# Kernel optimization log

Hardware: AMD Instinct MI355X
Metric: run time of the kernel (lower is better)

## Reference

```python
import jax, jax.numpy as jnp
import numpy as np

B = 16384          # batch_size
NF = 50            # n_fields
K = 16             # embedding_dim
V = 1_000_000      # input_dim (vocab)
H = 400            # fc hidden
NNZ = B * NF


def _xavier(key, shape):
    fan_in, fan_out = shape
    lim = (6.0 / (fan_in + fan_out)) ** 0.5
    return jax.random.uniform(key, shape, minval=-lim, maxval=lim, dtype=jnp.float32)


def setup_inputs() -> dict:
    key = jax.random.key(0)
    ks = jax.random.split(key, 12)
    feats = jax.random.randint(ks[0], (NNZ,), 0, V)
    # n_fields contiguous features per sample (required by view(batch_size,-1))
    index = jnp.repeat(jnp.arange(B), NF)
    values = jax.random.uniform(ks[1], (NNZ,), dtype=jnp.float32)
    bias = jnp.zeros((1, 1), jnp.float32)
    weights = _xavier(ks[2], (V, 1))
    embedding = _xavier(ks[3], (V, K))
    d = NF * K  # 800
    W0 = _xavier(ks[4], (d, H))
    b0 = jax.random.normal(ks[5], (1, 1), jnp.float32)
    W1 = _xavier(ks[6], (H, H))
    b1 = jax.random.normal(ks[7], (1, 1), jnp.float32)
    W2 = _xavier(ks[8], (H, 1))
    b2 = jax.random.normal(ks[9], (1, 1), jnp.float32)
    return dict(index=index, feats=feats, values=values, bias=bias,
                weights=weights, embedding=embedding,
                W0=W0, b0=b0, W1=W1, b1=b1, W2=W2, b2=b2, batch_size=B)


def reference(index, feats, values, bias, weights, embedding,
              W0, b0, W1, b1, W2, b2, batch_size):
    # gather (F.embedding)
    w = weights[feats, 0]              # [nnz]
    emb = embedding[feats]             # [nnz, K]

    # first order: segment-sum of w*v, plus bias ([B] + [1,1] -> [1,B], as in torch)
    first = jax.ops.segment_sum(w * values, index, num_segments=batch_size) + bias

    # second order: FM pooling trick, fused over all K dims in one segment reduce
    ev = emb * values[:, None]                                        # [nnz, K]
    s1 = jax.ops.segment_sum(ev, index, num_segments=batch_size)      # [B, K]
    s2 = jax.ops.segment_sum(ev * ev, index, num_segments=batch_size) # [B, K]
    second = 0.5 * jnp.sum(s1 * s1 - s2, axis=1)                      # [B]

    # higher order MLP (relu on every layer, scalar biases)
    x = emb.reshape(batch_size, -1)    # [B, NF*K]
    x = jax.nn.relu(x @ W0 + b0)
    x = jax.nn.relu(x @ W1 + b1)
    x = jax.nn.relu(x @ W2 + b2)       # [B, 1]
    higher = x.reshape(-1)             # [B]

    return jax.nn.sigmoid(first + second + higher)  # [1, B]
```

## Files before the change

kernel.cpp:

```cpp
#include <hip/hip_runtime.h>
#include <hip/hip_bf16.h>


#define BATCH 16384
#define NFLD  50
#define EK    16
#define DDIM  800
#define HDIM  400
#define HPAD  416
#define NPAD  512

typedef __attribute__((ext_vector_type(8))) __bf16 bf16x8;
typedef __attribute__((ext_vector_type(4))) float  f32x4;

typedef const __attribute__((address_space(1))) unsigned int* gas_u32p;
typedef __attribute__((address_space(3))) unsigned int*       las_u32p;

__device__ __forceinline__ void gld_lds16(const void* g, void* l) {
    __builtin_amdgcn_global_load_lds((gas_u32p)g, (las_u32p)l, 16, 0, 0);
}

__global__ __launch_bounds__(256) void transpose_pad_kernel(
    const float* __restrict__ src, __hip_bfloat16* __restrict__ dst,
    int srcK, int srcN, int dstCols)
{
    __shared__ float tile[32][33];
    const int tx = threadIdx.x & 31, ty = threadIdx.x >> 5;
    const int k0 = blockIdx.x * 32, n0 = blockIdx.y * 32;
#pragma unroll
    for (int r = 0; r < 4; ++r) {
        int k = k0 + ty + r * 8;
        int n = n0 + tx;
        float v = (k < srcK && n < srcN) ? src[(long)k * srcN + n] : 0.f;
        tile[ty + r * 8][tx] = v;
    }
    __syncthreads();
#pragma unroll
    for (int r = 0; r < 4; ++r) {
        int n = n0 + ty + r * 8;
        int k = k0 + tx;
        dst[(long)n * dstCols + k] = __float2bfloat16(tile[tx][ty + r * 8]);
    }
}

__global__ __launch_bounds__(256) void gather_fm_kernel(
    const int* __restrict__ feats, const float* __restrict__ values,
    const float* __restrict__ biasp, const float* __restrict__ weights,
    const float* __restrict__ embedding,
    float* __restrict__ fs, __hip_bfloat16* __restrict__ x)
{
    const int wave = threadIdx.x >> 6;
    const int lane = threadIdx.x & 63;
    const int s    = blockIdx.x * 4 + wave;
    const int r    = lane >> 2, c = lane & 3;
    const long base = (long)s * NFLD;

    int   f = 0; float v = 0.f, wsum = 0.f;
    if (lane < NFLD) {
        f = feats[base + lane];
        v = values[base + lane];
        wsum = weights[f] * v;
    }

    f32x4 s1 = {0.f, 0.f, 0.f, 0.f}, s2 = {0.f, 0.f, 0.f, 0.f};
#pragma unroll
    for (int p = 0; p < 4; ++p) {
        const int j = p * 16 + r;
        if (p < 3 || r < 2) {
            int   fj = __shfl(f, j);
            float vj = __shfl(v, j);
            const float4 e = *(const float4*)(embedding + (long)fj * EK + c * 4);
            f32x4 ef = {e.x, e.y, e.z, e.w};
            f32x4 ev = ef * vj;
            s1 += ev;
            s2 += ev * ev;
            __hip_bfloat16 pk[4] = {
                __float2bfloat16(e.x), __float2bfloat16(e.y),
                __float2bfloat16(e.z), __float2bfloat16(e.w)};
            *(uint2*)&x[(long)s * DDIM + j * EK + c * 4] = *(uint2*)pk;
        }
    }
#pragma unroll
    for (int m = 4; m <= 32; m <<= 1) {
        s1.x += __shfl_xor(s1.x, m); s1.y += __shfl_xor(s1.y, m);
        s1.z += __shfl_xor(s1.z, m); s1.w += __shfl_xor(s1.w, m);
        s2.x += __shfl_xor(s2.x, m); s2.y += __shfl_xor(s2.y, m);
        s2.z += __shfl_xor(s2.z, m); s2.w += __shfl_xor(s2.w, m);
    }
    float t = (s1.x * s1.x - s2.x) + (s1.y * s1.y - s2.y)
            + (s1.z * s1.z - s2.z) + (s1.w * s1.w - s2.w);
    t += __shfl_xor(t, 1); t += __shfl_xor(t, 2);
    wsum += __shfl_xor(wsum, 1);  wsum += __shfl_xor(wsum, 2);
    wsum += __shfl_xor(wsum, 4);  wsum += __shfl_xor(wsum, 8);
    wsum += __shfl_xor(wsum, 16); wsum += __shfl_xor(wsum, 32);
    if (lane == 0) fs[s] = wsum + 0.5f * t + biasp[0];
}

template <int KDIM, bool OUT_BF16, int LDC, bool PAD_OUT>
__global__ __launch_bounds__(256) void gemm_relu_kernel(
    const __hip_bfloat16* __restrict__ A,
    const __hip_bfloat16* __restrict__ Bt,
    const float* __restrict__ biasp,
    void* __restrict__ C)
{
    constexpr int KT = KDIM / 32;
    __shared__ __align__(16) __hip_bfloat16 sA[128 * 32];
    __shared__ __align__(16) __hip_bfloat16 sB[128 * 32];

    const int tid  = threadIdx.x;
    const int wave = tid >> 6, lane = tid & 63;
    const int l16  = lane & 15, quad = lane >> 4;
    const int waveM = wave & 1, waveN = wave >> 1;
    const int m0 = blockIdx.y * 128;
    const int n0 = blockIdx.x * 128;

    f32x4 acc[4][4] = {};

    const long ar0 = (long)(m0 + wave * 16 + (lane >> 2)) * KDIM;
    const long ar1 = ar0 + (long)64 * KDIM;
    const long br0 = (long)(n0 + wave * 16 + (lane >> 2)) * KDIM;
    const long br1 = br0 + (long)64 * KDIM;
    const int  ac  = (lane & 3) * 8;
    __hip_bfloat16* ldsA0 = sA + wave * 512 + lane * 8;
    __hip_bfloat16* ldsA1 = sA + 2048 + wave * 512 + lane * 8;
    __hip_bfloat16* ldsB0 = sB + wave * 512 + lane * 8;
    __hip_bfloat16* ldsB1 = sB + 2048 + wave * 512 + lane * 8;

    for (int kt = 0; kt < KT; ++kt) {
        const int k0 = kt * 32;
        gld_lds16(A  + ar0 + k0 + ac, ldsA0);
        gld_lds16(A  + ar1 + k0 + ac, ldsA1);
        gld_lds16(Bt + br0 + k0 + ac, ldsB0);
        gld_lds16(Bt + br1 + k0 + ac, ldsB1);
        __syncthreads();

        bf16x8 af[4], bfr[4];
#pragma unroll
        for (int i = 0; i < 4; ++i)
            af[i] = *(const bf16x8*)&sA[(waveM * 64 + i * 16 + l16) * 32 + quad * 8];
#pragma unroll
        for (int j = 0; j < 4; ++j)
            bfr[j] = *(const bf16x8*)&sB[(waveN * 64 + j * 16 + l16) * 32 + quad * 8];
#pragma unroll
        for (int i = 0; i < 4; ++i)
#pragma unroll
            for (int j = 0; j < 4; ++j)
                acc[i][j] = __builtin_amdgcn_mfma_f32_16x16x32_bf16(
                    af[i], bfr[j], acc[i][j], 0, 0, 0);
        __syncthreads();
    }

    const float bias = biasp[0];
#pragma unroll
    for (int i = 0; i < 4; ++i) {
        const int row = m0 + waveM * 64 + i * 16 + quad * 4;
#pragma unroll
        for (int j = 0; j < 4; ++j) {
            const int col = n0 + waveN * 64 + j * 16 + l16;
#pragma unroll
            for (int r = 0; r < 4; ++r) {
                float v = acc[i][j][r] + bias;
                v = v > 0.f ? v : 0.f;
                if constexpr (OUT_BF16) {
                    __hip_bfloat16* Cp = (__hip_bfloat16*)C;
                    if (col < HDIM)
                        Cp[(long)(row + r) * LDC + col] = __float2bfloat16(v);
                    else if (PAD_OUT && col < LDC)
                        Cp[(long)(row + r) * LDC + col] = __float2bfloat16(0.f);
                } else {
                    float* Cp = (float*)C;
                    if (col < HDIM)
                        Cp[(long)(row + r) * LDC + col] = v;
                }
            }
        }
    }
}

__global__ __launch_bounds__(256) void final_kernel(
    const float* __restrict__ h1, const float* __restrict__ W2,
    const float* __restrict__ b2p, const float* __restrict__ fs,
    float* __restrict__ out)
{
    const int wave = threadIdx.x >> 6, lane = threadIdx.x & 63;
    const int s = blockIdx.x * 4 + wave;
    const float* row = h1 + (long)s * HDIM;
    float acc;
    {
        float4 a = *(const float4*)(row + lane * 4);
        float4 w = *(const float4*)(W2 + lane * 4);
        acc = a.x * w.x + a.y * w.y + a.z * w.z + a.w * w.w;
    }
    if (lane < 36) {
        float4 a = *(const float4*)(row + 256 + lane * 4);
        float4 w = *(const float4*)(W2 + 256 + lane * 4);
        acc += a.x * w.x + a.y * w.y + a.z * w.z + a.w * w.w;
    }
    acc += __shfl_xor(acc, 32); acc += __shfl_xor(acc, 16);
    acc += __shfl_xor(acc, 8);  acc += __shfl_xor(acc, 4);
    acc += __shfl_xor(acc, 2);  acc += __shfl_xor(acc, 1);
    if (lane == 0) {
        float h = acc + b2p[0];
        h = h > 0.f ? h : 0.f;
        float z = fs[s] + h;
        out[s] = 1.f / (1.f + __expf(-z));
    }
}

extern "C" void kernel_launch(void* const* d_in, const int* in_sizes, int n_in,
                              void* d_out, int out_size, void* d_ws, size_t ws_size,
                              hipStream_t stream)
{
    const int*   feats     = (const int*)d_in[1];
    const float* values    = (const float*)d_in[2];
    const float* bias      = (const float*)d_in[3];
    const float* weights   = (const float*)d_in[4];
    const float* embedding = (const float*)d_in[5];
    const float* W0 = (const float*)d_in[6];
    const float* b0 = (const float*)d_in[7];
    const float* W1 = (const float*)d_in[8];
    const float* b1 = (const float*)d_in[9];
    const float* W2 = (const float*)d_in[10];
    const float* b2 = (const float*)d_in[11];

    char* ws = (char*)d_ws;
    size_t off = 0;
    auto alloc = [&](size_t bytes) {
        void* p = ws + off;
        off += (bytes + 255) & ~(size_t)255;
        return p;
    };
    float*          fs  = (float*)alloc((size_t)BATCH * 4);
    __hip_bfloat16* x   = (__hip_bfloat16*)alloc((size_t)BATCH * DDIM * 2);
    __hip_bfloat16* h0  = (__hip_bfloat16*)alloc((size_t)BATCH * HPAD * 2);
    float*          h1  = (float*)alloc((size_t)BATCH * HDIM * 4);
    __hip_bfloat16* W0t = (__hip_bfloat16*)alloc((size_t)NPAD * DDIM * 2);
    __hip_bfloat16* W1t = (__hip_bfloat16*)alloc((size_t)NPAD * HPAD * 2);
    (void)ws_size; (void)in_sizes; (void)n_in; (void)out_size;

    transpose_pad_kernel<<<dim3(DDIM / 32, NPAD / 32), 256, 0, stream>>>(
        W0, W0t, DDIM, HDIM, DDIM);
    transpose_pad_kernel<<<dim3(HPAD / 32, NPAD / 32), 256, 0, stream>>>(
        W1, W1t, HDIM, HDIM, HPAD);
    gather_fm_kernel<<<dim3(BATCH / 4), 256, 0, stream>>>(
        feats, values, bias, weights, embedding, fs, x);
    gemm_relu_kernel<DDIM, true, HPAD, true>
        <<<dim3(NPAD / 128, BATCH / 128), 256, 0, stream>>>(x, W0t, b0, (void*)h0);
    gemm_relu_kernel<HPAD, false, HDIM, false>
        <<<dim3(NPAD / 128, BATCH / 128), 256, 0, stream>>>(h0, W1t, b1, (void*)h1);
    final_kernel<<<dim3(BATCH / 4), 256, 0, stream>>>(
        h1, W2, b2, fs, (float*)d_out);
}
```

Measured before the change: 197.4 us.

## Fuse W2 projection into second GEMM epilogue and merge weight transposes

The second GEMM epilogue now applies bias and ReLU, multiplies by W2 and reduces across columns. It writes 8 partial sums per row instead of the full fp32 hidden activation, so the final kernel only sums the partials and applies the sigmoid. This removes writing and rereading the 16384x400 fp32 h1 buffer. The two weight-transpose launches are merged into one grid with a z dimension, and the gather kernel issues all embedding loads before consuming them to raise memory-level parallelism.

New measurement: 187.9 us. 4.8% less time.

```diff
diff --git a/kernel.cpp b/kernel.cpp
--- a/kernel.cpp
+++ b/kernel.cpp
@@ -21,9 +21,17 @@
 }
 
 __global__ __launch_bounds__(256) void transpose_pad_kernel(
-    const float* __restrict__ src, __hip_bfloat16* __restrict__ dst,
-    int srcK, int srcN, int dstCols)
-{
+    const float* __restrict__ W0, const float* __restrict__ W1,
+    __hip_bfloat16* __restrict__ W0t, __hip_bfloat16* __restrict__ W1t)
+{
+    const int which = blockIdx.z;
+    if (which == 1 && blockIdx.x >= HPAD / 32) return;
+    const float* src = which ? W1 : W0;
+    __hip_bfloat16* dst = which ? W1t : W0t;
+    const int srcK = which ? HDIM : DDIM;
+    const int srcN = HDIM;
+    const int dstCols = which ? HPAD : DDIM;
+
     __shared__ float tile[32][33];
     const int tx = threadIdx.x & 31, ty = threadIdx.x >> 5;
     const int k0 = blockIdx.x * 32, n0 = blockIdx.y * 32;
@@ -62,21 +70,30 @@
         wsum = weights[f] * v;
     }
 
+    int   fj[4]; float vj[4];
+#pragma unroll
+    for (int p = 0; p < 4; ++p) {
+        const int j = p * 16 + r;
+        if (p < 3 || r < 2) { fj[p] = __shfl(f, j); vj[p] = __shfl(v, j); }
+    }
+    float4 e[4];
+#pragma unroll
+    for (int p = 0; p < 4; ++p)
+        if (p < 3 || r < 2)
+            e[p] = *(const float4*)(embedding + (long)fj[p] * EK + c * 4);
+
     f32x4 s1 = {0.f, 0.f, 0.f, 0.f}, s2 = {0.f, 0.f, 0.f, 0.f};
 #pragma unroll
     for (int p = 0; p < 4; ++p) {
         const int j = p * 16 + r;
         if (p < 3 || r < 2) {
-            int   fj = __shfl(f, j);
-            float vj = __shfl(v, j);
-            const float4 e = *(const float4*)(embedding + (long)fj * EK + c * 4);
-            f32x4 ef = {e.x, e.y, e.z, e.w};
-            f32x4 ev = ef * vj;
+            f32x4 ef = {e[p].x, e[p].y, e[p].z, e[p].w};
+            f32x4 ev = ef * vj[p];
             s1 += ev;
             s2 += ev * ev;
             __hip_bfloat16 pk[4] = {
-                __float2bfloat16(e.x), __float2bfloat16(e.y),
-                __float2bfloat16(e.z), __float2bfloat16(e.w)};
+                __float2bfloat16(e[p].x), __float2bfloat16(e[p].y),
+                __float2bfloat16(e[p].z), __float2bfloat16(e[p].w)};
             *(uint2*)&x[(long)s * DDIM + j * EK + c * 4] = *(uint2*)pk;
         }
     }
@@ -96,11 +113,12 @@
     if (lane == 0) fs[s] = wsum + 0.5f * t + biasp[0];
 }
 
-template <int KDIM, bool OUT_BF16, int LDC, bool PAD_OUT>
+template <int KDIM, int MODE, int LDC>
 __global__ __launch_bounds__(256) void gemm_relu_kernel(
     const __hip_bfloat16* __restrict__ A,
     const __hip_bfloat16* __restrict__ Bt,
     const float* __restrict__ biasp,
+    const float* __restrict__ W2,
     void* __restrict__ C)
 {
     constexpr int KT = KDIM / 32;
@@ -151,60 +169,67 @@
     }
 
     const float bias = biasp[0];
-#pragma unroll
-    for (int i = 0; i < 4; ++i) {
-        const int row = m0 + waveM * 64 + i * 16 + quad * 4;
-#pragma unroll
-        for (int j = 0; j < 4; ++j) {
-            const int col = n0 + waveN * 64 + j * 16 + l16;
-#pragma unroll
-            for (int r = 0; r < 4; ++r) {
-                float v = acc[i][j][r] + bias;
-                v = v > 0.f ? v : 0.f;
-                if constexpr (OUT_BF16) {
+    if constexpr (MODE == 0) {
+#pragma unroll
+        for (int i = 0; i < 4; ++i) {
+            const int row = m0 + waveM * 64 + i * 16 + quad * 4;
+#pragma unroll
+            for (int j = 0; j < 4; ++j) {
+                const int col = n0 + waveN * 64 + j * 16 + l16;
+#pragma unroll
+                for (int r = 0; r < 4; ++r) {
+                    float v = acc[i][j][r] + bias;
+                    v = v > 0.f ? v : 0.f;
                     __hip_bfloat16* Cp = (__hip_bfloat16*)C;
                     if (col < HDIM)
                         Cp[(long)(row + r) * LDC + col] = __float2bfloat16(v);
-                    else if (PAD_OUT && col < LDC)
+                    else if (col < LDC)
                         Cp[(long)(row + r) * LDC + col] = __float2bfloat16(0.f);
-                } else {
-                    float* Cp = (float*)C;
-                    if (col < HDIM)
-                        Cp[(long)(row + r) * LDC + col] = v;
                 }
             }
         }
+    } else {
+        float w2v[4];
+#pragma unroll
+        for (int j = 0; j < 4; ++j) {
+            int col = n0 + waveN * 64 + j * 16 + l16;
+            w2v[j] = (col < HDIM) ? W2[col] : 0.f;
+        }
+        const int slot = blockIdx.x * 2 + waveN;
+#pragma unroll
+        for (int i = 0; i < 4; ++i) {
+#pragma unroll
+            for (int r = 0; r < 4; ++r) {
+                float p = 0.f;
+#pragma unroll
+                for (int j = 0; j < 4; ++j) {
+                    float v = acc[i][j][r] + bias;
+                    v = v > 0.f ? v : 0.f;
+                    p += v * w2v[j];
+                }
+                p += __shfl_xor(p, 1); p += __shfl_xor(p, 2);
+                p += __shfl_xor(p, 4); p += __shfl_xor(p, 8);
+                if (l16 == 0) {
+                    int row = m0 + waveM * 64 + i * 16 + quad * 4 + r;
+                    ((float*)C)[(long)row * 8 + slot] = p;
+                }
+            }
+        }
     }
 }
 
 __global__ __launch_bounds__(256) void final_kernel(
-    const float* __restrict__ h1, const float* __restrict__ W2,
-    const float* __restrict__ b2p, const float* __restrict__ fs,
-    float* __restrict__ out)
-{
-    const int wave = threadIdx.x >> 6, lane = threadIdx.x & 63;
-    const int s = blockIdx.x * 4 + wave;
-    const float* row = h1 + (long)s * HDIM;
-    float acc;
-    {
-        float4 a = *(const float4*)(row + lane * 4);
-        float4 w = *(const float4*)(W2 + lane * 4);
-        acc = a.x * w.x + a.y * w.y + a.z * w.z + a.w * w.w;
-    }
-    if (lane < 36) {
-        float4 a = *(const float4*)(row + 256 + lane * 4);
-        float4 w = *(const float4*)(W2 + 256 + lane * 4);
-        acc += a.x * w.x + a.y * w.y + a.z * w.z + a.w * w.w;
-    }
-    acc += __shfl_xor(acc, 32); acc += __shfl_xor(acc, 16);
-    acc += __shfl_xor(acc, 8);  acc += __shfl_xor(acc, 4);
-    acc += __shfl_xor(acc, 2);  acc += __shfl_xor(acc, 1);
-    if (lane == 0) {
-        float h = acc + b2p[0];
-        h = h > 0.f ? h : 0.f;
-        float z = fs[s] + h;
-        out[s] = 1.f / (1.f + __expf(-z));
-    }
+    const float* __restrict__ partial, const float* __restrict__ b2p,
+    const float* __restrict__ fs, float* __restrict__ out)
+{
+    const int s = blockIdx.x * 256 + threadIdx.x;
+    const float4 p0 = *(const float4*)(partial + (long)s * 8);
+    const float4 p1 = *(const float4*)(partial + (long)s * 8 + 4);
+    float sum = (p0.x + p0.y) + (p0.z + p0.w) + (p1.x + p1.y) + (p1.z + p1.w);
+    float h = sum + b2p[0];
+    h = h > 0.f ? h : 0.f;
+    float z = fs[s] + h;
+    out[s] = 1.f / (1.f + __expf(-z));
 }
 
 extern "C" void kernel_launch(void* const* d_in, const int* in_sizes, int n_in,
@@ -230,24 +255,24 @@
         off += (bytes + 255) & ~(size_t)255;
         return p;
     };
-    float*          fs  = (float*)alloc((size_t)BATCH * 4);
-    __hip_bfloat16* x   = (__hip_bfloat16*)alloc((size_t)BATCH * DDIM * 2);
-    __hip_bfloat16* h0  = (__hip_bfloat16*)alloc((size_t)BATCH * HPAD * 2);
-    float*          h1  = (float*)alloc((size_t)BATCH * HDIM * 4);
-    __hip_bfloat16* W0t = (__hip_bfloat16*)alloc((size_t)NPAD * DDIM * 2);
-    __hip_bfloat16* W1t = (__hip_bfloat16*)alloc((size_t)NPAD * HPAD * 2);
+    float*          fs   = (float*)alloc((size_t)BATCH * 4);
+    __hip_bfloat16* x    = (__hip_bfloat16*)alloc((size_t)BATCH * DDIM * 2);
+    __hip_bfloat16* h0   = (__hip_bfloat16*)alloc((size_t)BATCH * HPAD * 2);
+    float*          part = (float*)alloc((size_t)BATCH * 8 * 4);
+    __hip_bfloat16* W0t  = (__hip_bfloat16*)alloc((size_t)NPAD * DDIM * 2);
+    __hip_bfloat16* W1t  = (__hip_bfloat16*)alloc((size_t)NPAD * HPAD * 2);
     (void)ws_size; (void)in_sizes; (void)n_in; (void)out_size;
 
-    transpose_pad_kernel<<<dim3(DDIM / 32, NPAD / 32), 256, 0, stream>>>(
-        W0, W0t, DDIM, HDIM, DDIM);
-    transpose_pad_kernel<<<dim3(HPAD / 32, NPAD / 32), 256, 0, stream>>>(
-        W1, W1t, HDIM, HDIM, HPAD);
+    transpose_pad_kernel<<<dim3(DDIM / 32, NPAD / 32, 2), 256, 0, stream>>>(
+        W0, W1, W0t, W1t);
     gather_fm_kernel<<<dim3(BATCH / 4), 256, 0, stream>>>(
         feats, values, bias, weights, embedding, fs, x);
-    gemm_relu_kernel<DDIM, true, HPAD, true>
-        <<<dim3(NPAD / 128, BATCH / 128), 256, 0, stream>>>(x, W0t, b0, (void*)h0);
-    gemm_relu_kernel<HPAD, false, HDIM, false>
-        <<<dim3(NPAD / 128, BATCH / 128), 256, 0, stream>>>(h0, W1t, b1, (void*)h1);
-    final_kernel<<<dim3(BATCH / 4), 256, 0, stream>>>(
-        h1, W2, b2, fs, (float*)d_out);
-}
+    gemm_relu_kernel<DDIM, 0, HPAD>
+        <<<dim3(NPAD / 128, BATCH / 128), 256, 0, stream>>>(
+        x, W0t, b0, nullptr, (void*)h0);
+    gemm_relu_kernel<HPAD, 1, 8>
+        <<<dim3(NPAD / 128, BATCH / 128), 256, 0, stream>>>(
+        h0, W1t, b1, W2, (void*)part);
+    final_kernel<<<dim3(BATCH / 256), 256, 0, stream>>>(
+        part, b2, fs, (float*)d_out);
+}
```
